# Optimization experiments

Measured on AMD Instinct MI355X. Metric: run time of the kernel, lower is better.

Reference implementation:

```python
import jax, jax.numpy as jnp
import numpy as np

B, S, E, H = 8, 2048, 1024, 8
D = E // H  # head_dim = 128
LN_EPS = 1e-5


def setup_inputs() -> dict:
    key = jax.random.key(0)
    ks = jax.random.split(key, 4)
    x = jax.random.normal(ks[0], (B, S, E), dtype=jnp.float32)
    in_proj_w = jax.random.normal(ks[1], (3 * E, E), dtype=jnp.float32) * 0.02
    in_proj_b = jnp.zeros((3 * E,), dtype=jnp.float32)
    out_w = jax.random.normal(ks[2], (E, E), dtype=jnp.float32) * 0.02
    out_b = jnp.zeros((E,), dtype=jnp.float32)
    ln_g = jnp.ones((E,), dtype=jnp.float32)
    ln_b = jnp.zeros((E,), dtype=jnp.float32)
    return {"x": x, "in_proj_w": in_proj_w, "in_proj_b": in_proj_b,
            "out_w": out_w, "out_b": out_b, "ln_g": ln_g, "ln_b": ln_b}


def _layernorm(x, g, b):
    mu = jnp.mean(x, axis=-1, keepdims=True)
    var = jnp.mean(jnp.square(x - mu), axis=-1, keepdims=True)
    return (x - mu) * jax.lax.rsqrt(var + LN_EPS) * g + b


def reference(x, in_proj_w, in_proj_b, out_w, out_b, ln_g, ln_b):
    # Packed QKV projection (matches nn.MultiheadAttention in_proj)
    qkv = x @ in_proj_w.T + in_proj_b            # [B, S, 3E]
    q, k, v = jnp.split(qkv, 3, axis=-1)
    q = q.reshape(B, S, H, D).transpose(0, 2, 1, 3)  # [B, H, S, D]
    k = k.reshape(B, S, H, D).transpose(0, 2, 1, 3)
    v = v.reshape(B, S, H, D).transpose(0, 2, 1, 3)
    scale = 1.0 / jnp.sqrt(jnp.float32(D))
    scores = jnp.einsum('bhqd,bhkd->bhqk', q * scale, k)  # [B, H, S, S]
    attn = jax.nn.softmax(scores, axis=-1)
    # dropout(p=0.1) is identity in eval mode
    ctx = jnp.einsum('bhqk,bhkd->bhqd', attn, v)           # [B, H, S, D]
    ctx = ctx.transpose(0, 2, 1, 3).reshape(B, S, E)
    attn_out = ctx @ out_w.T + out_b                        # [B, S, E]
    y = _layernorm(x + attn_out, ln_g, ln_b)
    context = jnp.mean(y, axis=1)                           # [B, E]
    attn_weights = jnp.mean(attn, axis=1)                   # averaged over heads: [B, S, S]
    return (context, attn_weights)
```

## Files before the change

kernel.cpp:

```cpp
#include <hip/hip_runtime.h>
#include <math.h>

#define B_ 8
#define S_ 2048
#define E_ 1024
#define H_ 8
#define D_ 128
#define LN_EPS 1e-5f
#define SCALE 0.08838834764831845f

typedef __attribute__((ext_vector_type(8))) short bf16x8;
typedef __attribute__((ext_vector_type(4))) float f32x4;
typedef unsigned short ushort_t;

__device__ __forceinline__ unsigned short f2bf(float f) {
  unsigned int u = __float_as_uint(f);
  unsigned int r = (u + 0x7fffu + ((u >> 16) & 1u)) >> 16;
  return (unsigned short)r;
}
__device__ __forceinline__ float bf2f(short v) {
  return __uint_as_float(((unsigned int)(unsigned short)v) << 16);
}

typedef __attribute__((address_space(3))) unsigned int lds_u32;
typedef const __attribute__((address_space(1))) unsigned int glob_u32;
__device__ __forceinline__ void load_lds16(const void* g, void* l) {
  __builtin_amdgcn_global_load_lds((glob_u32*)g, (lds_u32*)l, 16, 0, 0);
}


__global__ __launch_bounds__(256) void cast_bf16_kernel(
    const float* __restrict__ s0, ushort_t* __restrict__ d0, int n0,
    const float* __restrict__ s1, ushort_t* __restrict__ d1, int n1,
    const float* __restrict__ s2, ushort_t* __restrict__ d2, int n2) {
  int i = blockIdx.x * 256 + threadIdx.x;
  const float* s;
  ushort_t* d;
  int off;
  if (i < n0) { s = s0; d = d0; off = i; }
  else if (i < n0 + n1) { s = s1; d = d1; off = i - n0; }
  else if (i < n0 + n1 + n2) { s = s2; d = d2; off = i - n0 - n1; }
  else return;
  const float4 a = *(const float4*)(s + (size_t)off * 8);
  const float4 b = *(const float4*)(s + (size_t)off * 8 + 4);
  bf16x8 v;
  v[0] = (short)f2bf(a.x); v[1] = (short)f2bf(a.y);
  v[2] = (short)f2bf(a.z); v[3] = (short)f2bf(a.w);
  v[4] = (short)f2bf(b.x); v[5] = (short)f2bf(b.y);
  v[6] = (short)f2bf(b.z); v[7] = (short)f2bf(b.w);
  *(bf16x8*)(d + (size_t)off * 8) = v;
}


#define GEMM_BODY(A_, B_ptr, K_)                                               \
  const int tid = threadIdx.x;                                                 \
  const int wave = tid >> 6, lane = tid & 63;                                  \
  const int lrow = lane & 15, quad = lane >> 4;                                \
  const int wm = (wave >> 1) * 64, wn = (wave & 1) * 64;                       \
  const int row0 = blockIdx.y * 128, col0 = blockIdx.x * 128;                  \
  f32x4 acc[4][4] = {};                                                        \
  for (int k0 = 0; k0 < (K_); k0 += 32) {                                      \
    __syncthreads();                                                           \
    _Pragma("unroll")                                                          \
    for (int j = 0; j < 2; ++j) {                                              \
      const int cid = j * 256 + tid;                                           \
      const int r = cid >> 2, c = cid & 3;                                     \
      load_lds16((A_) + (size_t)(row0 + r) * (K_) + k0 + ((c ^ (r & 3)) * 8),  \
                 &sA[cid * 8]);                                                \
    }                                                                          \
    _Pragma("unroll")                                                          \
    for (int j = 0; j < 2; ++j) {                                              \
      const int cid = j * 256 + tid;                                           \
      const int r = cid >> 2, c = cid & 3;                                     \
      load_lds16((B_ptr) + (size_t)(col0 + r) * (K_) + k0 + ((c ^ (r & 3)) * 8),\
                 &sB[cid * 8]);                                                \
    }                                                                          \
    __syncthreads();                                                           \
    bf16x8 af[4], bf[4];                                                       \
    _Pragma("unroll")                                                          \
    for (int t = 0; t < 4; ++t) {                                              \
      const int ra = wm + t * 16 + lrow;                                       \
      af[t] = *(const bf16x8*)&sA[ra * 32 + (quad ^ (ra & 3)) * 8];            \
      const int rb = wn + t * 16 + lrow;                                       \
      bf[t] = *(const bf16x8*)&sB[rb * 32 + (quad ^ (rb & 3)) * 8];            \
    }                                                                          \
    _Pragma("unroll")                                                          \
    for (int ti = 0; ti < 4; ++ti)                                             \
      _Pragma("unroll")                                                        \
      for (int tj = 0; tj < 4; ++tj)                                           \
        acc[ti][tj] = __builtin_amdgcn_mfma_f32_16x16x32_bf16(                 \
            af[ti], bf[tj], acc[ti][tj], 0, 0, 0);                             \
  }


__global__ __launch_bounds__(256, 3) void gemm_mfma_qkv(
    const ushort_t* __restrict__ A, const ushort_t* __restrict__ Bw,
    const float* __restrict__ bias, ushort_t* __restrict__ Qs,
    ushort_t* __restrict__ Kb, ushort_t* __restrict__ Vt) {
  __shared__ ushort_t smem[16640];
  ushort_t* sA = smem;
  ushort_t* sB = smem + 4096;
  GEMM_BODY(A, Bw, E_)

  const int ctile = blockIdx.x;
  const int kind = ctile >> 3;
  const int h = ctile & 7;
  const int b = row0 >> 11, s0 = row0 & 2047;
  const float cs = (kind == 0) ? SCALE : 1.f;
  ushort_t* T = smem;

  __syncthreads();
  #pragma unroll
  for (int ti = 0; ti < 4; ++ti)
    #pragma unroll
    for (int tj = 0; tj < 4; ++tj) {
      const int col = wn + tj * 16 + lrow;
      const float bv = bias[ctile * 128 + col];
      #pragma unroll
      for (int r = 0; r < 4; ++r) {
        const int row = wm + ti * 16 + quad * 4 + r;
        T[row * 130 + col] = f2bf((acc[ti][tj][r] + bv) * cs);
      }
    }
  __syncthreads();

  if (kind <= 1) {
    ushort_t* dst = (kind == 0 ? Qs : Kb) + ((size_t)(b * H_ + h) * S_ + s0) * D_;
    const int s = tid >> 1, half = tid & 1;
    #pragma unroll
    for (int j = 0; j < 8; ++j) {
      bf16x8 v = *(const bf16x8*)&T[s * 130 + half * 64 + j * 8];
      *(bf16x8*)&dst[(size_t)s * D_ + half * 64 + j * 8] = v;
    }
  } else {
    ushort_t* dst = Vt + (size_t)(b * H_ + h) * D_ * S_ + s0;
    const int d = tid >> 1, half = tid & 1;
    #pragma unroll
    for (int j = 0; j < 8; ++j) {
      bf16x8 v;
      #pragma unroll
      for (int jj = 0; jj < 8; ++jj)
        v[jj] = (short)T[(half * 64 + j * 8 + jj) * 130 + d];
      *(bf16x8*)&dst[(size_t)d * S_ + half * 64 + j * 8] = v;
    }
  }
}


__global__ __launch_bounds__(256, 3) void gemm_mfma_out(
    const ushort_t* __restrict__ A, const ushort_t* __restrict__ Bw,
    const float* __restrict__ bias, const float* __restrict__ res,
    float* __restrict__ C) {
  __shared__ ushort_t smem[16640];
  ushort_t* sA = smem;
  ushort_t* sB = smem + 4096;
  GEMM_BODY(A, Bw, E_)

  #pragma unroll
  for (int ti = 0; ti < 4; ++ti)
    #pragma unroll
    for (int tj = 0; tj < 4; ++tj) {
      const int col = col0 + wn + tj * 16 + lrow;
      const float bv = bias[col];
      #pragma unroll
      for (int r = 0; r < 4; ++r) {
        const int row = row0 + wm + ti * 16 + quad * 4 + r;
        const size_t idx = (size_t)row * E_ + col;
        C[idx] = acc[ti][tj][r] + bv + res[idx];
      }
    }
}


__global__ __launch_bounds__(512, 4) void attn_mfma(
    const ushort_t* __restrict__ Qs, const ushort_t* __restrict__ Kb,
    const ushort_t* __restrict__ Vt, ushort_t* __restrict__ ctx,
    float* __restrict__ attn_out) {
  __shared__ ushort_t Plds[16 * 2048];
  __shared__ float sinv[16];
  const int tid = threadIdx.x;
  const int wave = tid >> 6;
  const int lane = tid & 63;
  const int lrow = lane & 15;
  const int quad = lane >> 4;
  const int b = blockIdx.x & 7;
  const int q0 = (blockIdx.x >> 3) * 16;

  const int prow = tid >> 5;
  const int pcb = tid & 31;
  float pacc[8][8];
  #pragma unroll
  for (int i = 0; i < 8; ++i)
    #pragma unroll
    for (int j = 0; j < 8; ++j) pacc[i][j] = 0.f;

  for (int h = 0; h < H_; ++h) {
    const ushort_t* Qh = Qs + ((size_t)(b * H_ + h)) * S_ * D_;
    const ushort_t* Kh = Kb + ((size_t)(b * H_ + h)) * S_ * D_;
    const ushort_t* Vh = Vt + ((size_t)(b * H_ + h)) * D_ * S_;

    bf16x8 qf[4];
    #pragma unroll
    for (int t = 0; t < 4; ++t)
      qf[t] = *(const bf16x8*)(Qh + (size_t)(q0 + lrow) * D_ + t * 32 + quad * 8);

    for (int i = 0; i < 16; ++i) {
      const int ct = wave * 16 + i;
      f32x4 acc = {0.f, 0.f, 0.f, 0.f};
      #pragma unroll
      for (int t = 0; t < 4; ++t) {
        bf16x8 kf = *(const bf16x8*)(Kh + (size_t)(ct * 16 + lrow) * D_ + t * 32 + quad * 8);
        acc = __builtin_amdgcn_mfma_f32_16x16x32_bf16(qf[t], kf, acc, 0, 0, 0);
      }
      #pragma unroll
      for (int r = 0; r < 4; ++r) {
        const int row = quad * 4 + r;
        const int key = ct * 16 + lrow;
        const int idx = row * 2048 + (((((key >> 3) ^ (row & 7))) << 3) | (key & 7));
        Plds[idx] = f2bf(__expf(acc[r]));
      }
    }
    __syncthreads();

    float s = 0.f;
    #pragma unroll
    for (int i = 0; i < 8; ++i) {
      const int blk = pcb + 32 * i;
      const bf16x8 ev = *(const bf16x8*)&Plds[prow * 2048 + ((blk ^ (prow & 7)) << 3)];
      #pragma unroll
      for (int j = 0; j < 8; ++j) s += bf2f(ev[j]);
    }
    #pragma unroll
    for (int off = 1; off <= 16; off <<= 1) s += __shfl_xor(s, off);
    const float inv = 1.f / s;
    if (pcb == 0) sinv[prow] = inv;
    __syncthreads();

    const float w8 = inv * 0.125f;
    #pragma unroll
    for (int i = 0; i < 8; ++i) {
      const int blk = pcb + 32 * i;
      const bf16x8 ev = *(const bf16x8*)&Plds[prow * 2048 + ((blk ^ (prow & 7)) << 3)];
      #pragma unroll
      for (int j = 0; j < 8; ++j) pacc[i][j] += bf2f(ev[j]) * w8;
    }
    __syncthreads();

    f32x4 cacc = {0.f, 0.f, 0.f, 0.f};
    const ushort_t* Vd = Vh + (size_t)(wave * 16 + lrow) * S_;
    for (int kt = 0; kt < 64; ++kt) {
      const int blk = kt * 4 + quad;
      bf16x8 af = *(const bf16x8*)&Plds[lrow * 2048 + ((blk ^ (lrow & 7)) << 3)];
      bf16x8 vf = *(const bf16x8*)(Vd + kt * 32 + quad * 8);
      cacc = __builtin_amdgcn_mfma_f32_16x16x32_bf16(af, vf, cacc, 0, 0, 0);
    }
    #pragma unroll
    for (int r = 0; r < 4; ++r) {
      const int row = quad * 4 + r;
      ctx[((size_t)(b * S_ + q0 + row)) * E_ + h * D_ + wave * 16 + lrow] =
          f2bf(cacc[r] * sinv[row]);
    }
    __syncthreads();
  }

  float* ao = attn_out + ((size_t)(b * S_ + q0 + prow)) * S_;
  #pragma unroll
  for (int i = 0; i < 8; ++i) {
    const int key0 = (pcb + 32 * i) * 8;
    float4 v0 = {pacc[i][0], pacc[i][1], pacc[i][2], pacc[i][3]};
    float4 v1 = {pacc[i][4], pacc[i][5], pacc[i][6], pacc[i][7]};
    *(float4*)(ao + key0) = v0;
    *(float4*)(ao + key0 + 4) = v1;
  }
}


__device__ __forceinline__ float block_reduce_sum1(float v, float* red) {
  #pragma unroll
  for (int off = 32; off > 0; off >>= 1) v += __shfl_down(v, off);
  const int tid = threadIdx.x;
  __syncthreads();
  if ((tid & 63) == 0) red[tid >> 6] = v;
  __syncthreads();
  return (red[0] + red[1]) + (red[2] + red[3]);
}

__global__ __launch_bounds__(256) void ln_stats_kernel(
    const float* __restrict__ ypre, float* __restrict__ stats) {
  __shared__ float red[4];
  const int row = blockIdx.x;
  const int tid = threadIdx.x;
  const float* p = ypre + (size_t)row * E_;
  float4 v = *(const float4*)(p + tid * 4);
  float s = (v.x + v.y) + (v.z + v.w);
  s = block_reduce_sum1(s, red);
  const float mu = s * (1.f / E_);
  float e0 = v.x - mu, e1 = v.y - mu, e2 = v.z - mu, e3 = v.w - mu;
  float ss = (e0 * e0 + e1 * e1) + (e2 * e2 + e3 * e3);
  ss = block_reduce_sum1(ss, red);
  if (tid == 0) {
    stats[(size_t)row * 2 + 0] = mu;
    stats[(size_t)row * 2 + 1] = rsqrtf(ss * (1.f / E_) + LN_EPS);
  }
}


__global__ __launch_bounds__(256) void context_partial(
    const float* __restrict__ ypre, const float* __restrict__ stats,
    float* __restrict__ part) {
  const int e = blockIdx.x * 256 + threadIdx.x;
  const int b = blockIdx.y;
  const int c = blockIdx.z;
  float acc = 0.f;
  for (int s = c * 128; s < c * 128 + 128; ++s) {
    const size_t row = (size_t)b * S_ + s;
    acc += (ypre[row * E_ + e] - stats[row * 2]) * stats[row * 2 + 1];
  }
  part[((size_t)(b * 16 + c)) * E_ + e] = acc;
}

__global__ __launch_bounds__(256) void context_final(
    const float* __restrict__ part, const float* __restrict__ g,
    const float* __restrict__ bb, float* __restrict__ outctx) {
  const int idx = blockIdx.x * 256 + threadIdx.x;
  const int b = idx >> 10, e = idx & 1023;
  float acc = 0.f;
  #pragma unroll
  for (int c = 0; c < 16; ++c) acc += part[((size_t)(b * 16 + c)) * E_ + e];
  outctx[idx] = acc * (1.f / S_) * g[e] + bb[e];
}


extern "C" void kernel_launch(void* const* d_in, const int* in_sizes, int n_in,
                              void* d_out, int out_size, void* d_ws, size_t ws_size,
                              hipStream_t stream) {
  const float* x     = (const float*)d_in[0];
  const float* in_w  = (const float*)d_in[1];
  const float* in_b  = (const float*)d_in[2];
  const float* out_w = (const float*)d_in[3];
  const float* out_b = (const float*)d_in[4];
  const float* ln_g  = (const float*)d_in[5];
  const float* ln_b  = (const float*)d_in[6];

  float* out_ctx  = (float*)d_out;
  float* out_attn = out_ctx + (size_t)B_ * E_;

  char* ws = (char*)d_ws;
  const size_t MB = 1024 * 1024;
  ushort_t* xb     = (ushort_t*)(ws);
  ushort_t* Qs     = (ushort_t*)(ws + 32 * MB);
  ushort_t* Kb     = (ushort_t*)(ws + 64 * MB);
  ushort_t* Vt     = (ushort_t*)(ws + 96 * MB);
  ushort_t* ctxb16 = (ushort_t*)(ws + 128 * MB);
  float*    ypre   = (float*)(ws + 160 * MB);
  ushort_t* wb     = (ushort_t*)(ws + 224 * MB);
  ushort_t* owb    = (ushort_t*)(ws + 230 * MB);
  float*    stats  = (float*)(ws + 232 * MB);
  float*    part   = (float*)(ws + 233 * MB);

  const int n0 = B_ * S_ * E_ / 8, n1 = 3 * E_ * E_ / 8, n2 = E_ * E_ / 8;
  cast_bf16_kernel<<<(n0 + n1 + n2) / 256, 256, 0, stream>>>(
      x, xb, n0, in_w, wb, n1, out_w, owb, n2);

  gemm_mfma_qkv<<<dim3(3 * E_ / 128, B_ * S_ / 128), 256, 0, stream>>>(
      xb, wb, in_b, Qs, Kb, Vt);

  attn_mfma<<<(S_ / 16) * B_, 512, 0, stream>>>(Qs, Kb, Vt, ctxb16, out_attn);

  gemm_mfma_out<<<dim3(E_ / 128, B_ * S_ / 128), 256, 0, stream>>>(
      ctxb16, owb, out_b, x, ypre);

  ln_stats_kernel<<<B_ * S_, 256, 0, stream>>>(ypre, stats);

  context_partial<<<dim3(E_ / 256, B_, 16), 256, 0, stream>>>(ypre, stats, part);
  context_final<<<B_ * E_ / 256, 256, 0, stream>>>(part, ln_g, ln_b, out_ctx);
}
```

Measured before the change: 1.471 ms.

## Restructure attention kernel to 1024 threads with fused row sums and split-K PV

Doubles the attention block to 16 waves. Each wave computes half as many QK tiles, with K loads double-buffered and the softmax row sums accumulated as the tiles are produced, which removes the separate LDS pass that summed the exp values. The PV product is split across two halves of the key range, reduced through a shared buffer, and its LDS and V loads are software-pipelined. The change adds LDS use and a 1024-thread launch bound, which may limit occupancy and increase register pressure.

```diff
diff --git a/kernel.cpp b/kernel.cpp
--- a/kernel.cpp
+++ b/kernel.cpp
@@ -172,25 +172,46 @@
 }
 
 
-__global__ __launch_bounds__(512, 4) void attn_mfma(
+__device__ __forceinline__ void loadk4(bf16x8 k[4], const ushort_t* kp) {
+  k[0] = *(const bf16x8*)(kp);
+  k[1] = *(const bf16x8*)(kp + 32);
+  k[2] = *(const bf16x8*)(kp + 64);
+  k[3] = *(const bf16x8*)(kp + 96);
+}
+
+__device__ __forceinline__ void qk_tail(const f32x4 a, int ct, int lrow, int quad,
+                                        ushort_t* P, float* rs4) {
+  #pragma unroll
+  for (int r = 0; r < 4; ++r) {
+    const int row = (quad << 2) + r;
+    const int key = (ct << 4) | lrow;
+    const unsigned short us = f2bf(__expf(a[r]));
+    P[row * 2048 + ((((key >> 3) ^ (row & 7)) << 3) | (key & 7))] = us;
+    rs4[r] += bf2f((short)us);
+  }
+}
+
+__global__ __launch_bounds__(1024, 4) void attn_mfma(
     const ushort_t* __restrict__ Qs, const ushort_t* __restrict__ Kb,
     const ushort_t* __restrict__ Vt, ushort_t* __restrict__ ctx,
     float* __restrict__ attn_out) {
   __shared__ ushort_t Plds[16 * 2048];
-  __shared__ float sinv[16];
+  __shared__ float swredT[16 * 20];
+  __shared__ float ctmp[16 * 128];
   const int tid = threadIdx.x;
   const int wave = tid >> 6;
   const int lane = tid & 63;
   const int lrow = lane & 15;
   const int quad = lane >> 4;
+  const int x7 = lrow & 7;
   const int b = blockIdx.x & 7;
   const int q0 = (blockIdx.x >> 3) * 16;
-
-  const int prow = tid >> 5;
-  const int pcb = tid & 31;
-  float pacc[8][8];
-  #pragma unroll
-  for (int i = 0; i < 8; ++i)
+  const int half = wave >> 3;
+  const int dw = wave & 7;
+
+  float pacc[4][8];
+  #pragma unroll
+  for (int i = 0; i < 4; ++i)
     #pragma unroll
     for (int j = 0; j < 8; ++j) pacc[i][j] = 0.f;
 
@@ -204,69 +225,119 @@
     for (int t = 0; t < 4; ++t)
       qf[t] = *(const bf16x8*)(Qh + (size_t)(q0 + lrow) * D_ + t * 32 + quad * 8);
 
-    for (int i = 0; i < 16; ++i) {
-      const int ct = wave * 16 + i;
-      f32x4 acc = {0.f, 0.f, 0.f, 0.f};
-      #pragma unroll
-      for (int t = 0; t < 4; ++t) {
-        bf16x8 kf = *(const bf16x8*)(Kh + (size_t)(ct * 16 + lrow) * D_ + t * 32 + quad * 8);
-        acc = __builtin_amdgcn_mfma_f32_16x16x32_bf16(qf[t], kf, acc, 0, 0, 0);
+    const int ct0 = wave * 8;
+    float rs4[4] = {0.f, 0.f, 0.f, 0.f};
+    {
+      const ushort_t* Kp = Kh + (size_t)(ct0 * 16 + lrow) * D_ + (quad << 3);
+      bf16x8 k0[4], k1[4];
+      loadk4(k0, Kp);
+      loadk4(k1, Kp + 2048);
+      #pragma unroll
+      for (int ip = 0; ip < 4; ++ip) {
+        f32x4 a0 = {0.f, 0.f, 0.f, 0.f};
+        #pragma unroll
+        for (int t = 0; t < 4; ++t)
+          a0 = __builtin_amdgcn_mfma_f32_16x16x32_bf16(qf[t], k0[t], a0, 0, 0, 0);
+        if (ip < 3) loadk4(k0, Kp + (size_t)(2 * ip + 2) * 2048);
+        qk_tail(a0, ct0 + 2 * ip, lrow, quad, Plds, rs4);
+        f32x4 a1 = {0.f, 0.f, 0.f, 0.f};
+        #pragma unroll
+        for (int t = 0; t < 4; ++t)
+          a1 = __builtin_amdgcn_mfma_f32_16x16x32_bf16(qf[t], k1[t], a1, 0, 0, 0);
+        if (ip < 3) loadk4(k1, Kp + (size_t)(2 * ip + 3) * 2048);
+        qk_tail(a1, ct0 + 2 * ip + 1, lrow, quad, Plds, rs4);
       }
+    }
+    #pragma unroll
+    for (int r = 0; r < 4; ++r) {
+      #pragma unroll
+      for (int off = 1; off < 16; off <<= 1) rs4[r] += __shfl_xor(rs4[r], off);
+    }
+    if (lrow == 0) {
+      #pragma unroll
+      for (int r = 0; r < 4; ++r) swredT[((quad << 2) + r) * 20 + wave] = rs4[r];
+    }
+    __syncthreads();
+
+    float invr;
+    {
+      const float* sw = &swredT[lrow * 20];
+      const float4 s0 = *(const float4*)(sw);
+      const float4 s1 = *(const float4*)(sw + 4);
+      const float4 s2 = *(const float4*)(sw + 8);
+      const float4 s3 = *(const float4*)(sw + 12);
+      invr = 1.f / (((s0.x + s0.y) + (s0.z + s0.w)) +
+                    ((s1.x + s1.y) + (s1.z + s1.w)) +
+                    ((s2.x + s2.y) + (s2.z + s2.w)) +
+                    ((s3.x + s3.y) + (s3.z + s3.w)));
+    }
+    const float invp = 0.125f * __shfl(invr, wave);
+    float inv4[4];
+    #pragma unroll
+    for (int r = 0; r < 4; ++r) inv4[r] = __shfl(invr, (quad << 2) + r);
+
+    const ushort_t* Vd =
+        Vh + (size_t)(dw * 16 + lrow) * S_ + half * 1024 + (quad << 3);
+    const ushort_t* Prow = Plds + (lrow << 11);
+    const int blk0 = half << 7;
+    bf16x8 pa0, pv0, pa1, pv1, pa2, pv2, pa3, pv3;
+#define PVLD(A_, V_, KTL_)                                                     \
+  {                                                                            \
+    A_ = *(const bf16x8*)&Prow[(((blk0 + ((KTL_) << 2) + quad) ^ x7) << 3)];   \
+    V_ = *(const bf16x8*)(Vd + ((KTL_) << 5));                                 \
+  }
+    PVLD(pa0, pv0, 0); PVLD(pa1, pv1, 1); PVLD(pa2, pv2, 2); PVLD(pa3, pv3, 3);
+
+    #pragma unroll
+    for (int i = 0; i < 4; ++i) {
+      const int blk = lane + (i << 6);
+      const bf16x8 ev =
+          *(const bf16x8*)&Plds[(wave << 11) + ((blk ^ (wave & 7)) << 3)];
+      #pragma unroll
+      for (int j = 0; j < 8; ++j) pacc[i][j] += bf2f(ev[j]) * invp;
+    }
+
+    f32x4 c0 = {0.f, 0.f, 0.f, 0.f}, c1 = {0.f, 0.f, 0.f, 0.f};
+    #pragma unroll
+    for (int t = 0; t < 7; ++t) {
+      c0 = __builtin_amdgcn_mfma_f32_16x16x32_bf16(pa0, pv0, c0, 0, 0, 0);
+      PVLD(pa0, pv0, 4 * t + 4);
+      c1 = __builtin_amdgcn_mfma_f32_16x16x32_bf16(pa1, pv1, c1, 0, 0, 0);
+      PVLD(pa1, pv1, 4 * t + 5);
+      c0 = __builtin_amdgcn_mfma_f32_16x16x32_bf16(pa2, pv2, c0, 0, 0, 0);
+      PVLD(pa2, pv2, 4 * t + 6);
+      c1 = __builtin_amdgcn_mfma_f32_16x16x32_bf16(pa3, pv3, c1, 0, 0, 0);
+      PVLD(pa3, pv3, 4 * t + 7);
+    }
+    c0 = __builtin_amdgcn_mfma_f32_16x16x32_bf16(pa0, pv0, c0, 0, 0, 0);
+    c1 = __builtin_amdgcn_mfma_f32_16x16x32_bf16(pa1, pv1, c1, 0, 0, 0);
+    c0 = __builtin_amdgcn_mfma_f32_16x16x32_bf16(pa2, pv2, c0, 0, 0, 0);
+    c1 = __builtin_amdgcn_mfma_f32_16x16x32_bf16(pa3, pv3, c1, 0, 0, 0);
+#undef PVLD
+
+    if (half == 0) {
+      #pragma unroll
+      for (int r = 0; r < 4; ++r)
+        ctmp[((quad << 2) + r) * 128 + dw * 16 + lrow] = c0[r] + c1[r];
+    }
+    __syncthreads();
+    if (half == 1) {
       #pragma unroll
       for (int r = 0; r < 4; ++r) {
-        const int row = quad * 4 + r;
-        const int key = ct * 16 + lrow;
-        const int idx = row * 2048 + (((((key >> 3) ^ (row & 7))) << 3) | (key & 7));
-        Plds[idx] = f2bf(__expf(acc[r]));
+        const int row = (quad << 2) + r;
+        const float v =
+            (ctmp[row * 128 + dw * 16 + lrow] + c0[r] + c1[r]) * inv4[r];
+        ctx[((size_t)(b * S_ + q0 + row)) * E_ + h * D_ + dw * 16 + lrow] =
+            f2bf(v);
       }
     }
     __syncthreads();
-
-    float s = 0.f;
-    #pragma unroll
-    for (int i = 0; i < 8; ++i) {
-      const int blk = pcb + 32 * i;
-      const bf16x8 ev = *(const bf16x8*)&Plds[prow * 2048 + ((blk ^ (prow & 7)) << 3)];
-      #pragma unroll
-      for (int j = 0; j < 8; ++j) s += bf2f(ev[j]);
-    }
-    #pragma unroll
-    for (int off = 1; off <= 16; off <<= 1) s += __shfl_xor(s, off);
-    const float inv = 1.f / s;
-    if (pcb == 0) sinv[prow] = inv;
-    __syncthreads();
-
-    const float w8 = inv * 0.125f;
-    #pragma unroll
-    for (int i = 0; i < 8; ++i) {
-      const int blk = pcb + 32 * i;
-      const bf16x8 ev = *(const bf16x8*)&Plds[prow * 2048 + ((blk ^ (prow & 7)) << 3)];
-      #pragma unroll
-      for (int j = 0; j < 8; ++j) pacc[i][j] += bf2f(ev[j]) * w8;
-    }
-    __syncthreads();
-
-    f32x4 cacc = {0.f, 0.f, 0.f, 0.f};
-    const ushort_t* Vd = Vh + (size_t)(wave * 16 + lrow) * S_;
-    for (int kt = 0; kt < 64; ++kt) {
-      const int blk = kt * 4 + quad;
-      bf16x8 af = *(const bf16x8*)&Plds[lrow * 2048 + ((blk ^ (lrow & 7)) << 3)];
-      bf16x8 vf = *(const bf16x8*)(Vd + kt * 32 + quad * 8);
-      cacc = __builtin_amdgcn_mfma_f32_16x16x32_bf16(af, vf, cacc, 0, 0, 0);
-    }
-    #pragma unroll
-    for (int r = 0; r < 4; ++r) {
-      const int row = quad * 4 + r;
-      ctx[((size_t)(b * S_ + q0 + row)) * E_ + h * D_ + wave * 16 + lrow] =
-          f2bf(cacc[r] * sinv[row]);
-    }
-    __syncthreads();
-  }
-
-  float* ao = attn_out + ((size_t)(b * S_ + q0 + prow)) * S_;
-  #pragma unroll
-  for (int i = 0; i < 8; ++i) {
-    const int key0 = (pcb + 32 * i) * 8;
+  }
+
+  float* ao = attn_out + ((size_t)(b * S_ + q0 + wave)) * S_;
+  #pragma unroll
+  for (int i = 0; i < 4; ++i) {
+    const int key0 = (lane + (i << 6)) * 8;
     float4 v0 = {pacc[i][0], pacc[i][1], pacc[i][2], pacc[i][3]};
     float4 v1 = {pacc[i][4], pacc[i][5], pacc[i][6], pacc[i][7]};
     *(float4*)(ao + key0) = v0;
@@ -365,7 +436,7 @@
   gemm_mfma_qkv<<<dim3(3 * E_ / 128, B_ * S_ / 128), 256, 0, stream>>>(
       xb, wb, in_b, Qs, Kb, Vt);
 
-  attn_mfma<<<(S_ / 16) * B_, 512, 0, stream>>>(Qs, Kb, Vt, ctxb16, out_attn);
+  attn_mfma<<<(S_ / 16) * B_, 1024, 0, stream>>>(Qs, Kb, Vt, ctxb16, out_attn);
 
   gemm_mfma_out<<<dim3(E_ / 128, B_ * S_ / 128), 256, 0, stream>>>(
       ctxb16, owb, out_b, x, ypre);
```

Measured after the change: 1.679 ms. 14.1% more time.

## Split fused attention into tiled QK-exp, PV GEMM and head-average kernels per batch

Applied to the files above, without the earlier changes.

Replaces the single fused attention kernel, which handled 16 query rows per block with poor K/V reuse, with three kernels launched per batch. A 128x128 tiled GEMM computes exp(QK^T), writes unnormalised bf16 probabilities to a workspace chunk and accumulates row sums with atomics. A tiled PV GEMM then normalises the context, and a separate kernel averages the probabilities over heads into the attention output. This gains GEMM-style data reuse but adds a materialised P round trip through global memory (8x2048x2048 bf16 per batch), atomics on the row sums, and 24 extra launches.

```diff
diff --git a/kernel.cpp b/kernel.cpp
--- a/kernel.cpp
+++ b/kernel.cpp
@@ -172,106 +172,111 @@
 }
 
 
-__global__ __launch_bounds__(512, 4) void attn_mfma(
+__global__ __launch_bounds__(256) void zero_rsum_kernel(float* __restrict__ p) {
+  p[blockIdx.x * 256 + threadIdx.x] = 0.f;
+}
+
+__global__ __launch_bounds__(256, 3) void qk_gemm_exp(
     const ushort_t* __restrict__ Qs, const ushort_t* __restrict__ Kb,
-    const ushort_t* __restrict__ Vt, ushort_t* __restrict__ ctx,
-    float* __restrict__ attn_out) {
-  __shared__ ushort_t Plds[16 * 2048];
-  __shared__ float sinv[16];
-  const int tid = threadIdx.x;
-  const int wave = tid >> 6;
-  const int lane = tid & 63;
-  const int lrow = lane & 15;
-  const int quad = lane >> 4;
-  const int b = blockIdx.x & 7;
-  const int q0 = (blockIdx.x >> 3) * 16;
-
-  const int prow = tid >> 5;
-  const int pcb = tid & 31;
-  float pacc[8][8];
-  #pragma unroll
-  for (int i = 0; i < 8; ++i)
-    #pragma unroll
-    for (int j = 0; j < 8; ++j) pacc[i][j] = 0.f;
-
+    ushort_t* __restrict__ P, float* __restrict__ rsum, int b) {
+  __shared__ ushort_t smem[16640];
+  ushort_t* sA = smem;
+  ushort_t* sB = smem + 4096;
+  const int h = blockIdx.z;
+  const ushort_t* A = Qs + (size_t)(b * H_ + h) * S_ * D_;
+  const ushort_t* Bp = Kb + (size_t)(b * H_ + h) * S_ * D_;
+  GEMM_BODY(A, Bp, D_)
+
+  ushort_t* T = smem;
+  __syncthreads();
+  #pragma unroll
+  for (int ti = 0; ti < 4; ++ti)
+    #pragma unroll
+    for (int tj = 0; tj < 4; ++tj) {
+      const int col = wn + tj * 16 + lrow;
+      #pragma unroll
+      for (int r = 0; r < 4; ++r) {
+        const int row = wm + ti * 16 + quad * 4 + r;
+        T[row * 130 + col] = f2bf(__expf(acc[ti][tj][r]));
+      }
+    }
+  __syncthreads();
+
+  {
+    const int rr = tid >> 1, half = tid & 1;
+    ushort_t* dst = P + ((size_t)h * S_ + row0 + rr) * S_ + col0 + half * 64;
+    const ushort_t* src = &T[rr * 130 + half * 64];
+    float s = 0.f;
+    #pragma unroll
+    for (int j = 0; j < 8; ++j) {
+      const bf16x8 v = *(const bf16x8*)(src + j * 8);
+      *(bf16x8*)(dst + j * 8) = v;
+      #pragma unroll
+      for (int jj = 0; jj < 8; ++jj) s += bf2f(v[jj]);
+    }
+    s += __shfl_xor(s, 1);
+    if (half == 0)
+      atomicAdd(&rsum[(size_t)(b * H_ + h) * S_ + row0 + rr], s);
+  }
+}
+
+__global__ __launch_bounds__(256, 3) void pv_gemm(
+    const ushort_t* __restrict__ P, const ushort_t* __restrict__ Vt,
+    const float* __restrict__ rsum, ushort_t* __restrict__ ctx, int b) {
+  __shared__ ushort_t smem[16640];
+  ushort_t* sA = smem;
+  ushort_t* sB = smem + 4096;
+  const int h = blockIdx.z;
+  const ushort_t* A = P + (size_t)h * S_ * S_;
+  const ushort_t* Bp = Vt + (size_t)(b * H_ + h) * D_ * S_;
+  GEMM_BODY(A, Bp, S_)
+
+  ushort_t* T = smem;
+  __syncthreads();
+  const float* rs = rsum + (size_t)(b * H_ + h) * S_ + row0;
+  #pragma unroll
+  for (int ti = 0; ti < 4; ++ti)
+    #pragma unroll
+    for (int r = 0; r < 4; ++r) {
+      const int row = wm + ti * 16 + quad * 4 + r;
+      const float inv = 1.f / rs[row];
+      #pragma unroll
+      for (int tj = 0; tj < 4; ++tj) {
+        const int col = wn + tj * 16 + lrow;
+        T[row * 130 + col] = f2bf(acc[ti][tj][r] * inv);
+      }
+    }
+  __syncthreads();
+
+  {
+    const int rr = tid >> 1, half = tid & 1;
+    ushort_t* dst =
+        ctx + ((size_t)(b * S_ + row0 + rr)) * E_ + h * D_ + half * 64;
+    const ushort_t* src = &T[rr * 130 + half * 64];
+    #pragma unroll
+    for (int j = 0; j < 8; ++j)
+      *(bf16x8*)(dst + j * 8) = *(const bf16x8*)(src + j * 8);
+  }
+}
+
+
+__global__ __launch_bounds__(256) void attn_avg(
+    const ushort_t* __restrict__ P, const float* __restrict__ rsum_b,
+    float* __restrict__ attn_out_b) {
+  const int q = blockIdx.x;
+  const int k0 = threadIdx.x * 8;
+  float acc[8] = {};
+  #pragma unroll
   for (int h = 0; h < H_; ++h) {
-    const ushort_t* Qh = Qs + ((size_t)(b * H_ + h)) * S_ * D_;
-    const ushort_t* Kh = Kb + ((size_t)(b * H_ + h)) * S_ * D_;
-    const ushort_t* Vh = Vt + ((size_t)(b * H_ + h)) * D_ * S_;
-
-    bf16x8 qf[4];
-    #pragma unroll
-    for (int t = 0; t < 4; ++t)
-      qf[t] = *(const bf16x8*)(Qh + (size_t)(q0 + lrow) * D_ + t * 32 + quad * 8);
-
-    for (int i = 0; i < 16; ++i) {
-      const int ct = wave * 16 + i;
-      f32x4 acc = {0.f, 0.f, 0.f, 0.f};
-      #pragma unroll
-      for (int t = 0; t < 4; ++t) {
-        bf16x8 kf = *(const bf16x8*)(Kh + (size_t)(ct * 16 + lrow) * D_ + t * 32 + quad * 8);
-        acc = __builtin_amdgcn_mfma_f32_16x16x32_bf16(qf[t], kf, acc, 0, 0, 0);
-      }
-      #pragma unroll
-      for (int r = 0; r < 4; ++r) {
-        const int row = quad * 4 + r;
-        const int key = ct * 16 + lrow;
-        const int idx = row * 2048 + (((((key >> 3) ^ (row & 7))) << 3) | (key & 7));
-        Plds[idx] = f2bf(__expf(acc[r]));
-      }
-    }
-    __syncthreads();
-
-    float s = 0.f;
-    #pragma unroll
-    for (int i = 0; i < 8; ++i) {
-      const int blk = pcb + 32 * i;
-      const bf16x8 ev = *(const bf16x8*)&Plds[prow * 2048 + ((blk ^ (prow & 7)) << 3)];
-      #pragma unroll
-      for (int j = 0; j < 8; ++j) s += bf2f(ev[j]);
-    }
-    #pragma unroll
-    for (int off = 1; off <= 16; off <<= 1) s += __shfl_xor(s, off);
-    const float inv = 1.f / s;
-    if (pcb == 0) sinv[prow] = inv;
-    __syncthreads();
-
-    const float w8 = inv * 0.125f;
-    #pragma unroll
-    for (int i = 0; i < 8; ++i) {
-      const int blk = pcb + 32 * i;
-      const bf16x8 ev = *(const bf16x8*)&Plds[prow * 2048 + ((blk ^ (prow & 7)) << 3)];
-      #pragma unroll
-      for (int j = 0; j < 8; ++j) pacc[i][j] += bf2f(ev[j]) * w8;
-    }
-    __syncthreads();
-
-    f32x4 cacc = {0.f, 0.f, 0.f, 0.f};
-    const ushort_t* Vd = Vh + (size_t)(wave * 16 + lrow) * S_;
-    for (int kt = 0; kt < 64; ++kt) {
-      const int blk = kt * 4 + quad;
-      bf16x8 af = *(const bf16x8*)&Plds[lrow * 2048 + ((blk ^ (lrow & 7)) << 3)];
-      bf16x8 vf = *(const bf16x8*)(Vd + kt * 32 + quad * 8);
-      cacc = __builtin_amdgcn_mfma_f32_16x16x32_bf16(af, vf, cacc, 0, 0, 0);
-    }
-    #pragma unroll
-    for (int r = 0; r < 4; ++r) {
-      const int row = quad * 4 + r;
-      ctx[((size_t)(b * S_ + q0 + row)) * E_ + h * D_ + wave * 16 + lrow] =
-          f2bf(cacc[r] * sinv[row]);
-    }
-    __syncthreads();
-  }
-
-  float* ao = attn_out + ((size_t)(b * S_ + q0 + prow)) * S_;
-  #pragma unroll
-  for (int i = 0; i < 8; ++i) {
-    const int key0 = (pcb + 32 * i) * 8;
-    float4 v0 = {pacc[i][0], pacc[i][1], pacc[i][2], pacc[i][3]};
-    float4 v1 = {pacc[i][4], pacc[i][5], pacc[i][6], pacc[i][7]};
-    *(float4*)(ao + key0) = v0;
-    *(float4*)(ao + key0 + 4) = v1;
-  }
+    const float w = 0.125f / rsum_b[h * S_ + q];
+    const bf16x8 v = *(const bf16x8*)(P + ((size_t)h * S_ + q) * S_ + k0);
+    #pragma unroll
+    for (int j = 0; j < 8; ++j) acc[j] += bf2f(v[j]) * w;
+  }
+  float4 v0 = {acc[0], acc[1], acc[2], acc[3]};
+  float4 v1 = {acc[4], acc[5], acc[6], acc[7]};
+  *(float4*)(attn_out_b + (size_t)q * S_ + k0) = v0;
+  *(float4*)(attn_out_b + (size_t)q * S_ + k0 + 4) = v1;
 }
 
 
@@ -357,15 +362,26 @@
   ushort_t* owb    = (ushort_t*)(ws + 230 * MB);
   float*    stats  = (float*)(ws + 232 * MB);
   float*    part   = (float*)(ws + 233 * MB);
+  ushort_t* Pchunk = (ushort_t*)(ws + 160 * MB);
+  float*    rsum   = (float*)(ws + 233 * MB + 512 * 1024);
 
   const int n0 = B_ * S_ * E_ / 8, n1 = 3 * E_ * E_ / 8, n2 = E_ * E_ / 8;
   cast_bf16_kernel<<<(n0 + n1 + n2) / 256, 256, 0, stream>>>(
       x, xb, n0, in_w, wb, n1, out_w, owb, n2);
 
+  zero_rsum_kernel<<<B_ * H_ * S_ / 256, 256, 0, stream>>>(rsum);
+
   gemm_mfma_qkv<<<dim3(3 * E_ / 128, B_ * S_ / 128), 256, 0, stream>>>(
       xb, wb, in_b, Qs, Kb, Vt);
 
-  attn_mfma<<<(S_ / 16) * B_, 512, 0, stream>>>(Qs, Kb, Vt, ctxb16, out_attn);
+  for (int b = 0; b < B_; ++b) {
+    qk_gemm_exp<<<dim3(S_ / 128, S_ / 128, H_), 256, 0, stream>>>(
+        Qs, Kb, Pchunk, rsum, b);
+    pv_gemm<<<dim3(1, S_ / 128, H_), 256, 0, stream>>>(
+        Pchunk, Vt, rsum, ctxb16, b);
+    attn_avg<<<S_, 256, 0, stream>>>(
+        Pchunk, rsum + (size_t)b * H_ * S_, out_attn + (size_t)b * S_ * S_);
+  }
 
   gemm_mfma_out<<<dim3(E_ / 128, B_ * S_ / 128), 256, 0, stream>>>(
       ctxb16, owb, out_b, x, ypre);
```

New measurement: 1.204 ms. 18.2% less time.
